# Performance work log

Hardware: AMD Instinct MI355X
Metric: run time of the kernel (lower is better)

The kernel has to match this reference:

```python
import jax, jax.numpy as jnp
import numpy as np

ITEM_NUM = 50000
MAXLEN = 128
D_MODEL = 64
D_STATE = 32
D_CONV = 4
EXPAND = 2
D_INNER = EXPAND * D_MODEL  # 128
DT_RANK = max(1, -(-D_MODEL // 16))  # ceil(64/16) = 4
STD = 0.02


def setup_inputs() -> dict:
    key = jax.random.key(0)
    ks = jax.random.split(key, 12)
    B, L = 32, MAXLEN
    input_ids = jax.random.randint(ks[0], (B, L), 0, ITEM_NUM + 1)
    item_emb = STD * jax.random.normal(ks[1], (ITEM_NUM + 1, D_MODEL), jnp.float32)
    item_emb = item_emb.at[0].set(0.0)  # padding_idx=0 zeroed
    pos_emb = STD * jax.random.normal(ks[2], (MAXLEN, D_MODEL), jnp.float32)
    in_proj_w = STD * jax.random.normal(ks[3], (2 * D_INNER, D_MODEL), jnp.float32)
    conv_w = STD * jax.random.normal(ks[4], (D_INNER, D_CONV), jnp.float32)
    conv_b = jnp.zeros((D_INNER,), jnp.float32)
    x_proj_w = STD * jax.random.normal(ks[5], (DT_RANK + 2 * D_STATE, D_INNER), jnp.float32)
    dt_proj_w = STD * jax.random.normal(ks[6], (D_INNER, DT_RANK), jnp.float32)
    dt_proj_b = jnp.zeros((D_INNER,), jnp.float32)
    # A initialized as log of 1..d_state broadcast over channels (mamba_ssm S4D-real init)
    A_log = jnp.log(jnp.broadcast_to(jnp.arange(1, D_STATE + 1, dtype=jnp.float32), (D_INNER, D_STATE)))
    D_param = jnp.ones((D_INNER,), jnp.float32)
    out_proj_w = STD * jax.random.normal(ks[7], (D_MODEL, D_INNER), jnp.float32)
    return dict(input_ids=input_ids, item_emb=item_emb, pos_emb=pos_emb,
                in_proj_w=in_proj_w, conv_w=conv_w, conv_b=conv_b,
                x_proj_w=x_proj_w, dt_proj_w=dt_proj_w, dt_proj_b=dt_proj_b,
                A_log=A_log, D_param=D_param, out_proj_w=out_proj_w)


def _mamba_block(x, in_proj_w, conv_w, conv_b, x_proj_w, dt_proj_w, dt_proj_b, A_log, D_param, out_proj_w):
    B, L, _ = x.shape
    xz = jnp.einsum('bld,ed->ble', x, in_proj_w)  # (B,L,2*D_INNER)
    xc, z = jnp.split(xz, 2, axis=-1)
    # causal depthwise conv1d, kernel D_CONV, left-pad D_CONV-1
    xp = jnp.pad(xc, ((0, 0), (D_CONV - 1, 0), (0, 0)))
    xc = sum(xp[:, k:k + L, :] * conv_w[:, k] for k in range(D_CONV)) + conv_b
    xc = jax.nn.silu(xc)
    dbl = jnp.einsum('blc,ec->ble', xc, x_proj_w)
    dt, Bm, Cm = jnp.split(dbl, [DT_RANK, DT_RANK + D_STATE], axis=-1)
    delta = jax.nn.softplus(jnp.einsum('blr,cr->blc', dt, dt_proj_w) + dt_proj_b)  # (B,L,D_INNER)
    A = -jnp.exp(A_log)  # (D_INNER, D_STATE)
    dA = jnp.exp(delta[..., None] * A)                       # (B,L,C,S)
    dBu = delta[..., None] * Bm[:, :, None, :] * xc[..., None]  # (B,L,C,S)

    def step(h, inp):
        dA_t, dBu_t, C_t = inp  # (B,C,S),(B,C,S),(B,S)
        h = dA_t * h + dBu_t
        y = jnp.einsum('bcs,bs->bc', h, C_t)
        return h, y

    h0 = jnp.zeros((B, D_INNER, D_STATE), xc.dtype)
    _, ys = jax.lax.scan(step, h0, (dA.transpose(1, 0, 2, 3), dBu.transpose(1, 0, 2, 3), Cm.transpose(1, 0, 2)))
    y = ys.transpose(1, 0, 2) + D_param * xc  # (B,L,D_INNER)
    y = y * jax.nn.silu(z)
    return jnp.einsum('blc,dc->bld', y, out_proj_w)


def reference(input_ids, item_emb, pos_emb, in_proj_w, conv_w, conv_b,
              x_proj_w, dt_proj_w, dt_proj_b, A_log, D_param, out_proj_w):
    B, L = input_ids.shape
    seqs = item_emb[input_ids] * (D_MODEL ** 0.5)
    seqs = seqs + pos_emb[jnp.arange(L)][None, :, :]
    # dropout is identity in eval/deterministic mode
    pad_mask = (input_ids == 0)
    seqs = jnp.where(pad_mask[..., None], 0.0, seqs)
    seqs = _mamba_block(seqs, in_proj_w, conv_w, conv_b, x_proj_w,
                        dt_proj_w, dt_proj_b, A_log, D_param, out_proj_w)
    logits = jnp.einsum('bld,vd->blv', seqs, item_emb)  # matmul with item_emb.T
    return logits
```

## Files before the change

kernel.cpp:

```cpp
#include <hip/hip_runtime.h>
#include <math.h>

#define BB 32
#define LL 128
#define DM 64
#define DI 128
#define NV 50001
#define BL (BB*LL)
#define TM 32
#define TN 512
#define NT2 98
#define NPAD2 (NT2*TN)

typedef float f32x4 __attribute__((ext_vector_type(4)));
typedef _Float16 h16x8 __attribute__((ext_vector_type(8)));

__device__ __forceinline__ float silu_f(float x) { return x / (1.0f + expf(-x)); }

__global__ __launch_bounds__(512, 1) void k_pre(
    const int* __restrict__ ids, const float* __restrict__ item_emb,
    const float* __restrict__ pos_emb, const float* __restrict__ in_proj_w,
    const float* __restrict__ conv_w, const float* __restrict__ conv_b,
    const float* __restrict__ x_proj_w, const float* __restrict__ dt_proj_w,
    const float* __restrict__ dt_proj_b,
    float* __restrict__ zs_g, float* __restrict__ xcs_g,
    float* __restrict__ dbl_g, float* __restrict__ delta_g) {
    __shared__ float sq[19 * 68];
    __shared__ float px[19 * 132];
    __shared__ float cvS[16 * 132];
    __shared__ float dtS[16 * 4];
    const int t = threadIdx.x;
    const int bb = blockIdx.x >> 3, e8 = blockIdx.x & 7;
    const int T0 = e8 * 16;

    {
        int d = t & 63;
        for (int i = t >> 6; i < 19; i += 8) {
            int tl = T0 - 3 + i;
            float v = 0.f;
            if (tl >= 0) {
                int id = ids[bb * LL + tl];
                if (id != 0) v = item_emb[id * DM + d] * 8.0f + pos_emb[tl * DM + d];
            }
            sq[i * 68 + d] = v;
        }
    }
    __syncthreads();
    {
        int e = t & 255, half = t >> 8;
        f32x4 w4[16];
        const float* wr = in_proj_w + e * DM;
        #pragma unroll
        for (int k = 0; k < 16; k++) w4[k] = *(const f32x4*)&wr[4 * k];
        int i0 = half ? 10 : 0, i1 = half ? 19 : 10;
        for (int i = i0; i < i1; i++) {
            float a = 0.f;
            #pragma unroll
            for (int k = 0; k < 16; k++) {
                f32x4 s = *(const f32x4*)&sq[i * 68 + 4 * k];
                a += s.x * w4[k].x + s.y * w4[k].y + s.z * w4[k].z + s.w * w4[k].w;
            }
            if (e < 128) px[i * 132 + e] = a;
            else if (i >= 3) zs_g[(size_t)(bb * LL + T0 + i - 3) * DI + (e - 128)] = silu_f(a);
        }
    }
    __syncthreads();
    {
        int c = t & 127;
        float cw0 = conv_w[c * 4], cw1 = conv_w[c * 4 + 1];
        float cw2 = conv_w[c * 4 + 2], cw3 = conv_w[c * 4 + 3];
        float cb = conv_b[c];
        #pragma unroll
        for (int m = 0; m < 4; m++) {
            int j = 4 * m + (t >> 7);
            float v = silu_f(cb + px[j * 132 + c] * cw0 + px[(j + 1) * 132 + c] * cw1
                                + px[(j + 2) * 132 + c] * cw2 + px[(j + 3) * 132 + c] * cw3);
            cvS[j * 132 + c] = v;
            xcs_g[(size_t)(bb * LL + T0 + j) * DI + c] = v;
        }
    }
    __syncthreads();
    {
        int e = 4 + (t & 63), jg = t >> 6;
        f32x4 w4[32];
        const float* wr = x_proj_w + (size_t)e * DI;
        #pragma unroll
        for (int k = 0; k < 32; k++) w4[k] = *(const f32x4*)&wr[4 * k];
        #pragma unroll
        for (int jj = 0; jj < 2; jj++) {
            int j = jg + 8 * jj;
            float a = 0.f;
            #pragma unroll
            for (int k = 0; k < 32; k++) {
                f32x4 x = *(const f32x4*)&cvS[j * 132 + 4 * k];
                a += x.x * w4[k].x + x.y * w4[k].y + x.z * w4[k].z + x.w * w4[k].w;
            }
            dbl_g[(size_t)(bb * LL + T0 + j) * 64 + (e - 4)] = a;
        }
        if (t < 64) {
            int j2 = t >> 2, e2 = t & 3;
            const float* wr2 = x_proj_w + (size_t)e2 * DI;
            float a = 0.f;
            #pragma unroll
            for (int k = 0; k < 32; k++) {
                f32x4 x = *(const f32x4*)&cvS[j2 * 132 + 4 * k];
                f32x4 w2 = *(const f32x4*)&wr2[4 * k];
                a += x.x * w2.x + x.y * w2.y + x.z * w2.z + x.w * w2.w;
            }
            dtS[j2 * 4 + e2] = a;
        }
    }
    __syncthreads();
    {
        int c = t & 127;
        float dw0 = dt_proj_w[c * 4], dw1 = dt_proj_w[c * 4 + 1];
        float dw2 = dt_proj_w[c * 4 + 2], dw3 = dt_proj_w[c * 4 + 3];
        float db = dt_proj_b[c];
        #pragma unroll
        for (int m = 0; m < 4; m++) {
            int j = 4 * m + (t >> 7);
            float a = db + dtS[j * 4] * dw0 + dtS[j * 4 + 1] * dw1
                         + dtS[j * 4 + 2] * dw2 + dtS[j * 4 + 3] * dw3;
            float sp = (a > 20.f) ? a : log1pf(expf(a));
            delta_g[(size_t)(bb * LL + T0 + j) * DI + c] = sp;
        }
    }
}

__global__ __launch_bounds__(512, 1) void k_scan(
    const float* __restrict__ delta_g, const float* __restrict__ xcs_g,
    const float* __restrict__ dbl_g, const float* __restrict__ zs_g,
    const float* __restrict__ A_log, const float* __restrict__ Dp,
    float* __restrict__ y_g) {
    const int t = threadIdx.x;
    const int b = blockIdx.x >> 3, ce = blockIdx.x & 7;
    const int grp = t >> 5, s = t & 31;
    const int c = ce * 16 + grp;
    const size_t r0 = (size_t)(b * LL);
    float Acs = -expf(A_log[c * 32 + s]);
    float Dc = Dp[c];
    float h = 0.f;
    float Bt = dbl_g[r0 * 64 + s], Ct = dbl_g[r0 * 64 + 32 + s];
    float dlt = delta_g[r0 * DI + c], xct = xcs_g[r0 * DI + c];
    float zt = zs_g[r0 * DI + c];
    for (int tt = 0; tt < LL; tt++) {
        float Bn = 0.f, Cn = 0.f, zn = 0.f, dn = 0.f, xn = 0.f;
        if (tt < LL - 1) {
            size_t rn = r0 + tt + 1;
            Bn = dbl_g[rn * 64 + s]; Cn = dbl_g[rn * 64 + 32 + s];
            dn = delta_g[rn * DI + c]; xn = xcs_g[rn * DI + c];
            zn = zs_g[rn * DI + c];
        }
        h = expf(dlt * Acs) * h + (dlt * Bt) * xct;
        float p = h * Ct;
        #pragma unroll
        for (int off = 16; off; off >>= 1) p += __shfl_xor(p, off, 32);
        if (s == 0) y_g[(r0 + tt) * DI + c] = (p + Dc * xct) * zt;
        dlt = dn; xct = xn; Bt = Bn; Ct = Cn; zt = zn;
    }
}

__global__ __launch_bounds__(256, 2) void k_outproj(
    const float* __restrict__ y, const float* __restrict__ w,
    _Float16* __restrict__ outp_h) {
    __shared__ float ys[8 * 132];
    const int t = threadIdx.x;
    const int r0 = blockIdx.x * 8;
    {
        int r = t >> 5, c4 = t & 31;
        *(f32x4*)&ys[r * 132 + 4 * c4] = *(const f32x4*)&y[(size_t)(r0 + r) * DI + 4 * c4];
    }
    __syncthreads();
    int d = t & 63, rh = t >> 6;
    f32x4 w4[32];
    const float* wr = w + d * DI;
    #pragma unroll
    for (int k = 0; k < 32; k++) w4[k] = *(const f32x4*)&wr[4 * k];
    #pragma unroll
    for (int jj = 0; jj < 2; jj++) {
        int r = rh + 4 * jj;
        float a = 0.f;
        #pragma unroll
        for (int k = 0; k < 32; k++) {
            f32x4 x = *(const f32x4*)&ys[r * 132 + 4 * k];
            a += x.x * w4[k].x + x.y * w4[k].y + x.z * w4[k].z + x.w * w4[k].w;
        }
        outp_h[(size_t)(r0 + r) * 64 + d] = (_Float16)(a * 262144.0f);
    }
}

__global__ void k_cvt_emb(const float* __restrict__ emb, _Float16* __restrict__ embh) {
    int i = blockIdx.x * 256 + threadIdx.x;
    int r = i >> 6, d = i & 63;
    float v = (r < NV) ? emb[(size_t)r * 64 + d] * 1024.0f : 0.f;
    embh[i] = (_Float16)v;
}

__global__ __launch_bounds__(256, 2) void k_logits(
    const _Float16* __restrict__ A, const _Float16* __restrict__ Bm,
    float* __restrict__ logits) {
    __shared__ _Float16 As[TM * 72];
    __shared__ _Float16 Bs[TN * 72];
    const int m0 = blockIdx.x * TM;
    const int n0 = blockIdx.y * TN;
    const int t = threadIdx.x;

    {
        int r = t >> 3, c8 = t & 7;
        *(h16x8*)&As[r * 72 + c8 * 8] = *(const h16x8*)&A[(size_t)(m0 + r) * 64 + c8 * 8];
    }
    #pragma unroll
    for (int q = 0; q < 16; q++) {
        int idx = t + q * 256;
        int r = idx >> 3, c8 = idx & 7;
        *(h16x8*)&Bs[r * 72 + c8 * 8] = *(const h16x8*)&Bm[(size_t)(n0 + r) * 64 + c8 * 8];
    }
    __syncthreads();

    const int lane = t & 63, wv = t >> 6;
    const int lr = lane & 15, lg = lane >> 4;
    f32x4 acc[2][8];
    #pragma unroll
    for (int mi = 0; mi < 2; mi++)
        #pragma unroll
        for (int ni = 0; ni < 8; ni++)
            acc[mi][ni] = f32x4{0.f, 0.f, 0.f, 0.f};

    #pragma unroll
    for (int step = 0; step < 2; step++) {
        int kb = step * 32 + lg * 8;
        h16x8 a[2], b[8];
        #pragma unroll
        for (int mi = 0; mi < 2; mi++)
            a[mi] = *(const h16x8*)&As[(16 * mi + lr) * 72 + kb];
        #pragma unroll
        for (int ni = 0; ni < 8; ni++)
            b[ni] = *(const h16x8*)&Bs[(128 * wv + 16 * ni + lr) * 72 + kb];
        #pragma unroll
        for (int mi = 0; mi < 2; mi++)
            #pragma unroll
            for (int ni = 0; ni < 8; ni++)
                acc[mi][ni] = __builtin_amdgcn_mfma_f32_16x16x32_f16(a[mi], b[ni], acc[mi][ni], 0, 0, 0);
    }
    __syncthreads();

    float* Cs = (float*)Bs;
    const float SC = 3.7252902984619140625e-09f;
    #pragma unroll
    for (int mi = 0; mi < 2; mi++)
        #pragma unroll
        for (int ni = 0; ni < 8; ni++) {
            int col = 128 * wv + 16 * ni + lr;
            #pragma unroll
            for (int j = 0; j < 4; j++) {
                int row = 16 * mi + 4 * lg + j;
                Cs[row * 517 + col] = acc[mi][ni][j] * SC;
            }
        }
    __syncthreads();

    #pragma unroll
    for (int q = 0; q < 16; q++) {
        int r = 2 * q + (t >> 7);
        int c = t & 127;
        int grow = m0 + r;
        int s = (4 - (grow & 3)) & 3;
        float* dst = logits + (size_t)grow * NV + n0;
        const float* src = Cs + r * 517;
        if (s == 0) {
            int col = 4 * c;
            int gc = n0 + col;
            if (gc + 3 < NV) {
                __builtin_nontemporal_store(*(const f32x4*)&src[col], (f32x4*)&dst[col]);
            } else {
                #pragma unroll
                for (int e = 0; e < 4; e++)
                    if (gc + e < NV) __builtin_nontemporal_store(src[col + e], &dst[col + e]);
            }
        } else {
            if (c == 0) {
                for (int e = 0; e < s; e++)
                    if (n0 + e < NV) __builtin_nontemporal_store(src[e], &dst[e]);
            }
            if (c < 127) {
                int col = s + 4 * c;
                int gc = n0 + col;
                if (gc + 3 < NV) {
                    __builtin_nontemporal_store(*(const f32x4*)&src[col], (f32x4*)&dst[col]);
                } else {
                    #pragma unroll
                    for (int e = 0; e < 4; e++)
                        if (gc + e < NV) __builtin_nontemporal_store(src[col + e], &dst[col + e]);
                }
            } else {
                for (int e = s + 508; e < 512; e++)
                    if (n0 + e < NV) __builtin_nontemporal_store(src[e], &dst[e]);
            }
        }
    }
}

extern "C" void kernel_launch(void* const* d_in, const int* in_sizes, int n_in,
                              void* d_out, int out_size, void* d_ws, size_t ws_size,
                              hipStream_t stream) {
    const int*   ids       = (const int*)  d_in[0];
    const float* item_emb  = (const float*)d_in[1];
    const float* pos_emb   = (const float*)d_in[2];
    const float* in_proj_w = (const float*)d_in[3];
    const float* conv_w    = (const float*)d_in[4];
    const float* conv_b    = (const float*)d_in[5];
    const float* x_proj_w  = (const float*)d_in[6];
    const float* dt_proj_w = (const float*)d_in[7];
    const float* dt_proj_b = (const float*)d_in[8];
    const float* A_log     = (const float*)d_in[9];
    const float* Dp        = (const float*)d_in[10];
    const float* out_proj_w= (const float*)d_in[11];
    float* logits = (float*)d_out;

    float* ws     = (float*)d_ws;
    float* zs     = ws;
    float* xcs    = zs + (size_t)BL * DI;
    float* dblg   = xcs + (size_t)BL * DI;
    float* deltag = dblg + (size_t)BL * 64;
    float* yg     = deltag + (size_t)BL * DI;
    _Float16* outph = (_Float16*)(yg + (size_t)BL * DI);
    _Float16* embh  = outph + (size_t)BL * 64;

    k_cvt_emb<<<(NPAD2 * 64) / 256, 256, 0, stream>>>(item_emb, embh);
    k_pre<<<256, 512, 0, stream>>>(ids, item_emb, pos_emb, in_proj_w, conv_w, conv_b,
                                   x_proj_w, dt_proj_w, dt_proj_b,
                                   zs, xcs, dblg, deltag);
    k_scan<<<256, 512, 0, stream>>>(deltag, xcs, dblg, zs, A_log, Dp, yg);
    k_outproj<<<BL / 8, 256, 0, stream>>>(yg, out_proj_w, outph);
    dim3 lgd(BL / TM, NT2);
    k_logits<<<lgd, 256, 0, stream>>>(outph, embh, logits);
}
```

Measured before the change: 366.2 us.

## Fuse output projection into logits kernel, recomputing per tile

```diff
diff --git a/kernel.cpp b/kernel.cpp
--- a/kernel.cpp
+++ b/kernel.cpp
@@ -160,35 +160,6 @@
     }
 }
 
-__global__ __launch_bounds__(256, 2) void k_outproj(
-    const float* __restrict__ y, const float* __restrict__ w,
-    _Float16* __restrict__ outp_h) {
-    __shared__ float ys[8 * 132];
-    const int t = threadIdx.x;
-    const int r0 = blockIdx.x * 8;
-    {
-        int r = t >> 5, c4 = t & 31;
-        *(f32x4*)&ys[r * 132 + 4 * c4] = *(const f32x4*)&y[(size_t)(r0 + r) * DI + 4 * c4];
-    }
-    __syncthreads();
-    int d = t & 63, rh = t >> 6;
-    f32x4 w4[32];
-    const float* wr = w + d * DI;
-    #pragma unroll
-    for (int k = 0; k < 32; k++) w4[k] = *(const f32x4*)&wr[4 * k];
-    #pragma unroll
-    for (int jj = 0; jj < 2; jj++) {
-        int r = rh + 4 * jj;
-        float a = 0.f;
-        #pragma unroll
-        for (int k = 0; k < 32; k++) {
-            f32x4 x = *(const f32x4*)&ys[r * 132 + 4 * k];
-            a += x.x * w4[k].x + x.y * w4[k].y + x.z * w4[k].z + x.w * w4[k].w;
-        }
-        outp_h[(size_t)(r0 + r) * 64 + d] = (_Float16)(a * 262144.0f);
-    }
-}
-
 __global__ void k_cvt_emb(const float* __restrict__ emb, _Float16* __restrict__ embh) {
     int i = blockIdx.x * 256 + threadIdx.x;
     int r = i >> 6, d = i & 63;
@@ -197,18 +168,41 @@
 }
 
 __global__ __launch_bounds__(256, 2) void k_logits(
-    const _Float16* __restrict__ A, const _Float16* __restrict__ Bm,
-    float* __restrict__ logits) {
+    const float* __restrict__ y, const float* __restrict__ wo,
+    const _Float16* __restrict__ Bm, float* __restrict__ logits) {
     __shared__ _Float16 As[TM * 72];
     __shared__ _Float16 Bs[TN * 72];
     const int m0 = blockIdx.x * TM;
     const int n0 = blockIdx.y * TN;
     const int t = threadIdx.x;
 
-    {
-        int r = t >> 3, c8 = t & 7;
-        *(h16x8*)&As[r * 72 + c8 * 8] = *(const h16x8*)&A[(size_t)(m0 + r) * 64 + c8 * 8];
-    }
+    float* ys = (float*)Bs;
+    #pragma unroll
+    for (int q = 0; q < 4; q++) {
+        int idx = t + q * 256;
+        int r = idx >> 5, c4 = idx & 31;
+        *(f32x4*)&ys[r * 132 + 4 * c4] = *(const f32x4*)&y[(size_t)(m0 + r) * DI + 4 * c4];
+    }
+    __syncthreads();
+    {
+        int d = t & 63, rq = t >> 6;
+        f32x4 w4[32];
+        const float* wr = wo + (size_t)d * DI;
+        #pragma unroll
+        for (int k = 0; k < 32; k++) w4[k] = *(const f32x4*)&wr[4 * k];
+        #pragma unroll
+        for (int jj = 0; jj < 8; jj++) {
+            int r = rq + 4 * jj;
+            float a = 0.f;
+            #pragma unroll
+            for (int k = 0; k < 32; k++) {
+                f32x4 x = *(const f32x4*)&ys[r * 132 + 4 * k];
+                a += x.x * w4[k].x + x.y * w4[k].y + x.z * w4[k].z + x.w * w4[k].w;
+            }
+            As[r * 72 + d] = (_Float16)(a * 262144.0f);
+        }
+    }
+    __syncthreads();
     #pragma unroll
     for (int q = 0; q < 16; q++) {
         int idx = t + q * 256;
@@ -323,15 +317,13 @@
     float* dblg   = xcs + (size_t)BL * DI;
     float* deltag = dblg + (size_t)BL * 64;
     float* yg     = deltag + (size_t)BL * DI;
-    _Float16* outph = (_Float16*)(yg + (size_t)BL * DI);
-    _Float16* embh  = outph + (size_t)BL * 64;
+    _Float16* embh  = (_Float16*)(yg + (size_t)BL * DI);
 
     k_cvt_emb<<<(NPAD2 * 64) / 256, 256, 0, stream>>>(item_emb, embh);
     k_pre<<<256, 512, 0, stream>>>(ids, item_emb, pos_emb, in_proj_w, conv_w, conv_b,
                                    x_proj_w, dt_proj_w, dt_proj_b,
                                    zs, xcs, dblg, deltag);
     k_scan<<<256, 512, 0, stream>>>(deltag, xcs, dblg, zs, A_log, Dp, yg);
-    k_outproj<<<BL / 8, 256, 0, stream>>>(yg, out_proj_w, outph);
     dim3 lgd(BL / TM, NT2);
-    k_logits<<<lgd, 256, 0, stream>>>(outph, embh, logits);
-}
+    k_logits<<<lgd, 256, 0, stream>>>(yg, out_proj_w, embh, logits);
+}
```

Result: slower. 567.3 us (+54.9%).
